# Optimization experiments

Hardware: AMD Instinct MI355X
Metric: run time of the kernel (lower is better)

The kernel has to match this reference:

```python
import jax, jax.numpy as jnp
import numpy as np

N_NODES = 100000
EMB = 256
HID = 64
N_REL = 5
N_EDGES = 3200000
BATCH = 16384


def _rgcn_conv(x, W, root, b, src, dst, etype):
    # PyG RGCNConv with mean aggregation per relation:
    # out_i = sum_r mean_{j in N_r(i)} x_j @ W_r + x_i @ root + b
    N = x.shape[0]
    R = W.shape[0]
    h = jnp.einsum('ni,rio->rno', x, W)          # [R, N, O] per-relation transforms
    m = h[etype, src]                            # [E, O] per-edge messages
    seg = dst * R + etype                        # combined (node, relation) segment id
    sums = jax.ops.segment_sum(m, seg, num_segments=N * R)
    cnt = jax.ops.segment_sum(jnp.ones((m.shape[0],), dtype=x.dtype), seg,
                              num_segments=N * R)
    mean = sums / jnp.maximum(cnt, 1.0)[:, None]
    agg = mean.reshape(N, R, -1).sum(axis=1)     # sum over relations
    return agg + x @ root + b


def _merge(x1, x2, w1, b1, w2, b2):
    x = jnp.concatenate([x1, x2], axis=1)
    h = jax.nn.relu(x @ w1 + b1)
    return h @ w2 + b2                           # [B, 1] logits


def setup_inputs() -> dict:
    key = jax.random.key(0)
    ks = jax.random.split(key, 16)
    d = {}
    d['bill_id'] = jax.random.randint(ks[0], (BATCH,), 0, N_NODES)
    d['user1_id'] = jax.random.randint(ks[1], (BATCH,), 0, N_NODES)
    d['user2_id'] = jax.random.randint(ks[2], (BATCH,), 0, N_NODES)
    d['edge_index'] = jax.random.randint(ks[3], (2, N_EDGES), 0, N_NODES)
    d['edge_type'] = jax.random.randint(ks[4], (N_EDGES,), 0, N_REL)
    # learned params (xavier-ish scaling); linear weights stored as [in, out]
    d['users_feature'] = jax.random.normal(ks[5], (N_NODES, EMB), jnp.float32) * 0.06
    d['W1'] = jax.random.normal(ks[6], (N_REL, EMB, HID), jnp.float32) * 0.08
    d['root1'] = jax.random.normal(ks[7], (EMB, HID), jnp.float32) * 0.08
    d['b1'] = jnp.zeros((HID,), jnp.float32)
    d['W2'] = jax.random.normal(ks[8], (N_REL, HID, HID), jnp.float32) * 0.12
    d['root2'] = jax.random.normal(ks[9], (HID, HID), jnp.float32) * 0.12
    d['b2'] = jnp.zeros((HID,), jnp.float32)
    d['mfc1_w'] = jax.random.normal(ks[10], (2 * HID, HID), jnp.float32) * 0.1
    d['mfc1_b'] = jnp.zeros((HID,), jnp.float32)
    d['mfc2_w'] = jax.random.normal(ks[11], (HID, 1), jnp.float32) * 0.17
    d['mfc2_b'] = jnp.zeros((1,), jnp.float32)
    return d


def reference(bill_id, user1_id, user2_id, edge_index, edge_type,
              users_feature, W1, root1, b1, W2, root2, b2,
              mfc1_w, mfc1_b, mfc2_w, mfc2_b):
    src, dst = edge_index[0], edge_index[1]
    x = jax.nn.relu(_rgcn_conv(users_feature, W1, root1, b1, src, dst, edge_type))
    nodes = _rgcn_conv(x, W2, root2, b2, src, dst, edge_type)  # [N, 64]
    bill = nodes[bill_id]
    u1 = nodes[user1_id]
    u2 = nodes[user2_id]
    pos = _merge(bill, u1, mfc1_w, mfc1_b, mfc2_w, mfc2_b)  # [B, 1]
    neg = _merge(bill, u2, mfc1_w, mfc1_b, mfc2_w, mfc2_b)
    z = jnp.concatenate([pos, neg], axis=0)
    t = jnp.concatenate([jnp.ones_like(pos), jnp.zeros_like(pos)], axis=0)
    # numerically stable BCE-with-logits, mean reduction
    bce = jnp.mean(jnp.maximum(z, 0.0) - z * t + jnp.log1p(jnp.exp(-jnp.abs(z))))
    pred = jnp.round(jax.nn.sigmoid(z))
    acc = jnp.mean((pred == t).astype(jnp.float32))
    return (bce, acc)
```

## Files before the change

### kernel.cpp

```cpp
#include <hip/hip_runtime.h>
#include <hip/hip_bf16.h>

#define N_NODES 100000
#define EMB 256
#define HID 64
#define N_REL 5
#define N_EDGES 3200000
#define BATCH 16384
#define NB 782
#define NWG1 256
#define CH 12500
#define LSEG 640
#define NSEG (N_NODES * N_REL)

typedef unsigned short u16;
typedef unsigned int u32;
typedef __attribute__((ext_vector_type(4))) float f32x4;
typedef __attribute__((ext_vector_type(8))) short short8;

__device__ __forceinline__ float bf2f(u16 u) {
    union { float f; u32 i; } v;
    v.i = ((u32)u) << 16;
    return v.f;
}
__device__ __forceinline__ u16 f2bf(float f) {
    union { float f; u32 i; } v;
    v.f = f;
    u32 r = v.i + 0x7fff + ((v.i >> 16) & 1);
    return (u16)(r >> 16);
}

__device__ __forceinline__ void gload_lds16(const void* g, void* l) {
    __builtin_amdgcn_global_load_lds(
        (const __attribute__((address_space(1))) unsigned int*)g,
        (__attribute__((address_space(3))) unsigned int*)l, 16, 0, 0);
}

__global__ __launch_bounds__(256) void bucket_hist(const int* __restrict__ dst,
                                                   int* __restrict__ hist) {
    __shared__ int hl[NB];
    const int tid = threadIdx.x;
    for (int i = tid; i < NB; i += 256) hl[i] = 0;
    __syncthreads();
    const int w = blockIdx.x;
    const int s = w * CH, e = s + CH;
    for (int i = s + tid; i < e; i += 256)
        atomicAdd(&hl[dst[i] >> 7], 1);
    __syncthreads();
    for (int i = tid; i < NB; i += 256) hist[w * NB + i] = hl[i];
}

__global__ void col_scan(int* __restrict__ hist, int* __restrict__ btot) {
    const int b = blockIdx.x;
    const int lane = threadIdx.x;
    int carry = 0;
    for (int c = 0; c < NWG1; c += 64) {
        int v = hist[(c + lane) * NB + b];
        int incl = v;
#pragma unroll
        for (int off = 1; off < 64; off <<= 1) {
            int t = __shfl_up(incl, off);
            if (lane >= off) incl += t;
        }
        hist[(c + lane) * NB + b] = carry + (incl - v);
        carry += __shfl(incl, 63);
    }
    if (lane == 0) btot[b] = carry;
}

__global__ void btot_scan(const int* __restrict__ btot, int* __restrict__ boffs,
                          int* __restrict__ offs) {
    const int lane = threadIdx.x;
    int carry = 0;
    for (int c = 0; c < NB; c += 64) {
        int v = (c + lane < NB) ? btot[c + lane] : 0;
        int incl = v;
#pragma unroll
        for (int off = 1; off < 64; off <<= 1) {
            int t = __shfl_up(incl, off);
            if (lane >= off) incl += t;
        }
        if (c + lane < NB) boffs[c + lane] = carry + (incl - v);
        carry += __shfl(incl, 63);
    }
    if (lane == 0) {
        boffs[NB] = N_EDGES;
        offs[NSEG] = N_EDGES;
    }
}

__global__ __launch_bounds__(256) void bucket_scatter(
        const int* __restrict__ src, const int* __restrict__ dst,
        const int* __restrict__ et, const int* __restrict__ base,
        const int* __restrict__ boffs, u32* __restrict__ bucketed) {
    __shared__ int cur[NB];
    const int tid = threadIdx.x;
    const int w = blockIdx.x;
    for (int i = tid; i < NB; i += 256) cur[i] = boffs[i] + base[w * NB + i];
    __syncthreads();
    const int s = w * CH, e = s + CH;
    for (int i = s + tid; i < e; i += 256) {
        int d = dst[i];
        int b = d >> 7;
        u32 key = (u32)src[i] | ((u32)((d & 127) * 5 + et[i]) << 17);
        int pos = atomicAdd(&cur[b], 1);
        bucketed[pos] = key;
    }
}

__global__ __launch_bounds__(256) void seg_sort(
        const u32* __restrict__ keys, const int* __restrict__ boffs,
        int* __restrict__ offs, u32* __restrict__ soff) {
    __shared__ int cntl[LSEG];
    __shared__ int cur[LSEG];
    const int tid = threadIdx.x;
    const int b = blockIdx.x;
    const int s = boffs[b], e = boffs[b + 1];

    for (int i = tid; i < LSEG; i += 256) cntl[i] = 0;
    __syncthreads();
    for (int i = s + tid; i < e; i += 256)
        atomicAdd(&cntl[keys[i] >> 17], 1);
    __syncthreads();

    if (tid < 64) {
        int carry = 0;
        for (int c = 0; c < LSEG; c += 64) {
            int v = cntl[c + tid];
            int incl = v;
#pragma unroll
            for (int off = 1; off < 64; off <<= 1) {
                int t = __shfl_up(incl, off);
                if (tid >= off) incl += t;
            }
            cur[c + tid] = carry + (incl - v);
            carry += __shfl(incl, 63);
        }
    }
    __syncthreads();

    const int segbase = b * LSEG;
    for (int i = tid; i < LSEG; i += 256)
        if (segbase + i < NSEG) offs[segbase + i] = s + cur[i];
    __syncthreads();

    for (int i = s + tid; i < e; i += 256) {
        u32 key = keys[i];
        u32 lseg = key >> 17;
        int pos = s + atomicAdd(&cur[lseg], 1);
        u32 q = (lseg * 52429u) >> 18;
        u32 rel = lseg - q * 5u;
        soff[pos] = (key & 0x1FFFF) * 384u + rel * 64u;
    }
}

__global__ void build_bt(const float* __restrict__ W, const float* __restrict__ root,
                         int K, u16* __restrict__ BT) {
    int idx = blockIdx.x * blockDim.x + threadIdx.x;
    if (idx >= 384 * K) return;
    int j = idx / K, k = idx - j * K;
    float v = (j < 320) ? W[((j >> 6) * K + k) * 64 + (j & 63)]
                        : root[k * 64 + (j & 63)];
    BT[idx] = f2bf(v);
}

template <int K, bool A_F32>
__global__ __launch_bounds__(256) void mfma_gemm(
        const void* __restrict__ Av, const u16* __restrict__ BT,
        u16* __restrict__ C) {
    __shared__ __align__(16) u16 Al[128 * 64];
    __shared__ __align__(16) u16 Bl[128 * 64];
    const int tid  = threadIdx.x;
    const int lane = tid & 63;
    const int wave = tid >> 6;
    const int m0 = blockIdx.x * 128;
    const int n0 = blockIdx.y * 128;
    const int wr = (wave >> 1) * 64;
    const int wc = (wave & 1) * 64;
    const int l15 = lane & 15;
    const int lg  = lane >> 4;

    f32x4 acc[4][4];
#pragma unroll
    for (int i = 0; i < 4; ++i)
#pragma unroll
        for (int j = 0; j < 4; ++j) {
            f32x4 z = {0.f, 0.f, 0.f, 0.f};
            acc[i][j] = z;
        }

    for (int k0 = 0; k0 < K; k0 += 64) {
#pragma unroll
        for (int i = 0; i < 4; ++i) {
            int c = wave * 4 + i;
            int row = c * 8 + (lane >> 3);
            int kk  = (lane & 7) * 8;
            gload_lds16(BT + (size_t)(n0 + row) * K + k0 + kk, &Bl[c * 512]);
        }
        if (A_F32) {
            const float* Af = (const float*)Av;
#pragma unroll
            for (int p = 0; p < 8; ++p) {
                int f = p * 1024 + tid * 4;
                int row = f >> 6;
                int col = f & 63;
                int gr = m0 + row;
                if (gr > N_NODES - 1) gr = N_NODES - 1;
                float4 v = *(const float4*)(Af + (size_t)gr * K + k0 + col);
                ushort4 o;
                o.x = f2bf(v.x); o.y = f2bf(v.y); o.z = f2bf(v.z); o.w = f2bf(v.w);
                *(ushort4*)&Al[row * 64 + col] = o;
            }
        } else {
            const u16* Ab = (const u16*)Av;
#pragma unroll
            for (int i = 0; i < 4; ++i) {
                int c = wave * 4 + i;
                int row = c * 8 + (lane >> 3);
                int kk  = (lane & 7) * 8;
                gload_lds16(Ab + (size_t)(m0 + row) * K + k0 + kk, &Al[c * 512]);
            }
        }
        __syncthreads();

#pragma unroll
        for (int kk = 0; kk < 64; kk += 32) {
            short8 af[4], bf[4];
#pragma unroll
            for (int f = 0; f < 4; ++f) {
                af[f] = *(const short8*)&Al[(wr + f * 16 + l15) * 64 + kk + lg * 8];
                bf[f] = *(const short8*)&Bl[(wc + f * 16 + l15) * 64 + kk + lg * 8];
            }
#pragma unroll
            for (int fm = 0; fm < 4; ++fm)
#pragma unroll
                for (int fn = 0; fn < 4; ++fn)
                    acc[fm][fn] = __builtin_amdgcn_mfma_f32_16x16x32_bf16(
                        af[fm], bf[fn], acc[fm][fn], 0, 0, 0);
        }
        __syncthreads();
    }

#pragma unroll
    for (int fm = 0; fm < 4; ++fm) {
        int rbase = m0 + wr + fm * 16 + lg * 4;
#pragma unroll
        for (int i = 0; i < 4; ++i) {
            int r = rbase + i;
            if (r < N_NODES) {
#pragma unroll
                for (int fn = 0; fn < 4; ++fn)
                    C[(size_t)r * 384 + n0 + wc + fn * 16 + l15] = f2bf(acc[fm][fn][i]);
            }
        }
    }
}

template <bool RELU>
__global__ __launch_bounds__(256) void agg_rl(
        const u16* __restrict__ h, const u32* __restrict__ soff,
        const int* __restrict__ offs, const float* __restrict__ bias,
        u16* __restrict__ out) {
    const int lane = threadIdx.x & 63;
    const int d = (blockIdx.x * blockDim.x + threadIdx.x) >> 6;
    if (d >= N_NODES) return;

    const int o0 = offs[d * 5 + 0], o1 = offs[d * 5 + 1], o2 = offs[d * 5 + 2];
    const int o3 = offs[d * 5 + 3], o4 = offs[d * 5 + 4], o5 = offs[d * 5 + 5];
    const float i0 = 1.f / (float)max(o1 - o0, 1);
    const float i1 = 1.f / (float)max(o2 - o1, 1);
    const float i2 = 1.f / (float)max(o3 - o2, 1);
    const float i3 = 1.f / (float)max(o4 - o3, 1);
    const float i4 = 1.f / (float)max(o5 - o4, 1);

    const u16* hl = h + lane;
    float acc0 = bf2f(h[(size_t)d * 384 + 320 + lane]) + bias[lane];
    float acc1 = 0.f;

    for (int base = o0; base < o5; base += 64) {
        const int idx = base + lane;
        const u32 voff = soff[min(idx, o5 - 1)];
        float wv = idx < o1 ? i0 : idx < o2 ? i1 : idx < o3 ? i2
                 : idx < o4 ? i3 : i4;
        if (idx >= o5) wv = 0.f;
        const int m = min(64, o5 - base);
        for (int j = 0; j < m; j += 8) {
#pragma unroll
            for (int jj = 0; jj < 8; jj += 2) {
                int  offa = __builtin_amdgcn_readlane((int)voff, j + jj);
                int  wa_i = __builtin_amdgcn_readlane((int)__float_as_uint(wv), j + jj);
                int  offb = __builtin_amdgcn_readlane((int)voff, j + jj + 1);
                int  wb_i = __builtin_amdgcn_readlane((int)__float_as_uint(wv), j + jj + 1);
                acc0 += bf2f(hl[(u32)offa]) * __uint_as_float((u32)wa_i);
                acc1 += bf2f(hl[(u32)offb]) * __uint_as_float((u32)wb_i);
            }
        }
    }
    float acc = acc0 + acc1;
    if (RELU) acc = fmaxf(acc, 0.f);
    out[(size_t)d * 64 + lane] = f2bf(acc);
}

__global__ __launch_bounds__(256) void loss_kernel(
        const u16* __restrict__ nodes, const int* __restrict__ bill,
        const int* __restrict__ u1, const int* __restrict__ u2,
        const float* __restrict__ w1, const float* __restrict__ b1,
        const float* __restrict__ w2, const float* __restrict__ b2,
        float* __restrict__ out) {
    __shared__ float Wl[128 * 64];
    __shared__ float red[2][4];
    for (int j = threadIdx.x; j < 128 * 16; j += 256)
        ((float4*)Wl)[j] = ((const float4*)w1)[j];
    __syncthreads();

    const int lane = threadIdx.x & 63;
    const int wv   = threadIdx.x >> 6;
    const int gw   = blockIdx.x * 4 + wv;
    const int nw   = gridDim.x * 4;

    const float bias1 = b1[lane];
    const float w2l   = w2[lane];
    const float bias2 = b2[0];

    float bce_acc = 0.f, corr_acc = 0.f;
    for (int s = gw; s < BATCH; s += nw) {
        const u16* xb  = nodes + (size_t)bill[s] * 64;
        const u16* xu1 = nodes + (size_t)u1[s] * 64;
        const u16* xu2 = nodes + (size_t)u2[s] * 64;
        float hb = bias1, h1 = 0.f, h2 = 0.f;
#pragma unroll 8
        for (int i = 0; i < 64; ++i) {
            float wb = Wl[i * 64 + lane];
            float wu = Wl[(64 + i) * 64 + lane];
            hb += bf2f(xb[i]) * wb;
            h1 += bf2f(xu1[i]) * wu;
            h2 += bf2f(xu2[i]) * wu;
        }
        float p1 = fmaxf(hb + h1, 0.f) * w2l;
        float p2 = fmaxf(hb + h2, 0.f) * w2l;
#pragma unroll
        for (int off = 32; off > 0; off >>= 1) {
            p1 += __shfl_down(p1, off);
            p2 += __shfl_down(p2, off);
        }
        if (lane == 0) {
            float z1 = p1 + bias2;
            float z2 = p2 + bias2;
            bce_acc += fmaxf(z1, 0.f) - z1 + log1pf(expf(-fabsf(z1)));
            bce_acc += fmaxf(z2, 0.f)      + log1pf(expf(-fabsf(z2)));
            corr_acc += (z1 > 0.f) ? 1.f : 0.f;
            corr_acc += (z2 > 0.f) ? 0.f : 1.f;
        }
    }
    if (lane == 0) { red[0][wv] = bce_acc; red[1][wv] = corr_acc; }
    __syncthreads();
    if (threadIdx.x == 0) {
        const float scale = 1.f / (2.f * BATCH);
        atomicAdd(&out[0], (red[0][0] + red[0][1] + red[0][2] + red[0][3]) * scale);
        atomicAdd(&out[1], (red[1][0] + red[1][1] + red[1][2] + red[1][3]) * scale);
    }
}

extern "C" void kernel_launch(void* const* d_in, const int* in_sizes, int n_in,
                              void* d_out, int out_size, void* d_ws, size_t ws_size,
                              hipStream_t stream) {
    const int*   bill  = (const int*)d_in[0];
    const int*   u1    = (const int*)d_in[1];
    const int*   u2    = (const int*)d_in[2];
    const int*   ei    = (const int*)d_in[3];
    const int*   et    = (const int*)d_in[4];
    const float* uf    = (const float*)d_in[5];
    const float* W1    = (const float*)d_in[6];
    const float* root1 = (const float*)d_in[7];
    const float* b1    = (const float*)d_in[8];
    const float* W2    = (const float*)d_in[9];
    const float* root2 = (const float*)d_in[10];
    const float* b2    = (const float*)d_in[11];
    const float* m1w   = (const float*)d_in[12];
    const float* m1b   = (const float*)d_in[13];
    const float* m2w   = (const float*)d_in[14];
    const float* m2b   = (const float*)d_in[15];
    float* out = (float*)d_out;

    char* ws = (char*)d_ws;
    u16* h_all    = (u16*)(ws);
    u32* sorted   = (u32*)(ws + 76800000);
    u32* bucketed = (u32*)(ws + 89600000);
    u16* xbuf     = (u16*)(ws + 89600000);
    int* hist     = (int*)(ws + 102400000);
    int* btot     = (int*)(ws + 103200768);
    int* boffs    = (int*)(ws + 103203896);
    int* offs     = (int*)(ws + 103207040);
    u16* BT1      = (u16*)(ws + 105207056);
    u16* BT2      = (u16*)(ws + 105403664);
    if (ws_size < 105452816) return;

    const int* src = ei;
    const int* dst = ei + N_EDGES;

    hipMemsetAsync(d_out, 0, 2 * sizeof(float), stream);

    bucket_hist<<<NWG1, 256, 0, stream>>>(dst, hist);
    col_scan<<<NB, 64, 0, stream>>>(hist, btot);
    btot_scan<<<1, 64, 0, stream>>>(btot, boffs, offs);
    bucket_scatter<<<NWG1, 256, 0, stream>>>(src, dst, et, hist, boffs, bucketed);
    seg_sort<<<NB, 256, 0, stream>>>(bucketed, boffs, offs, sorted);

    build_bt<<<(384 * EMB + 255) / 256, 256, 0, stream>>>(W1, root1, EMB, BT1);
    build_bt<<<(384 * HID + 255) / 256, 256, 0, stream>>>(W2, root2, HID, BT2);

    mfma_gemm<EMB, true><<<dim3(782, 3), 256, 0, stream>>>(uf, BT1, h_all);
    agg_rl<true><<<25000, 256, 0, stream>>>(h_all, sorted, offs, b1, xbuf);

    mfma_gemm<HID, false><<<dim3(782, 3), 256, 0, stream>>>(xbuf, BT2, h_all);
    agg_rl<false><<<25000, 256, 0, stream>>>(h_all, sorted, offs, b2, xbuf);

    loss_kernel<<<1024, 256, 0, stream>>>(xbuf, bill, u1, u2, m1w, m1b, m2w, m2b, out);
}
```

Before: 371.3 us.

## Compute full 384-column output per block and XOR-swizzle LDS tiles

The GEMM now has each 512-thread block compute all 384 output columns for its 128 rows, replacing the 3-way column-tiled grid. The A tile (the fp32 user features in layer 1) is therefore read and converted to bf16 once per row tile instead of three times. LDS rows are XOR-swizzled to cut bank conflicts on the MFMA fragment loads, and the fp32 A load now uses wider per-thread loads packed into 8-wide bf16 stores. In exchange, each block uses much more LDS and more accumulator registers per wave, which may reduce occupancy.

```diff
diff --git a/kernel.cpp b/kernel.cpp
--- a/kernel.cpp
+++ b/kernel.cpp
@@ -29,6 +29,14 @@
     u32 r = v.i + 0x7fff + ((v.i >> 16) & 1);
     return (u16)(r >> 16);
 }
+__device__ __forceinline__ short8 pack8(float4 a, float4 b) {
+    short8 r;
+    r[0] = (short)f2bf(a.x); r[1] = (short)f2bf(a.y);
+    r[2] = (short)f2bf(a.z); r[3] = (short)f2bf(a.w);
+    r[4] = (short)f2bf(b.x); r[5] = (short)f2bf(b.y);
+    r[6] = (short)f2bf(b.z); r[7] = (short)f2bf(b.w);
+    return r;
+}
 
 __device__ __forceinline__ void gload_lds16(const void* g, void* l) {
     __builtin_amdgcn_global_load_lds(
@@ -165,76 +173,76 @@
 }
 
 template <int K, bool A_F32>
-__global__ __launch_bounds__(256) void mfma_gemm(
+__global__ __launch_bounds__(512) void gemm384(
         const void* __restrict__ Av, const u16* __restrict__ BT,
         u16* __restrict__ C) {
     __shared__ __align__(16) u16 Al[128 * 64];
-    __shared__ __align__(16) u16 Bl[128 * 64];
+    __shared__ __align__(16) u16 Bl[384 * 64];
     const int tid  = threadIdx.x;
     const int lane = tid & 63;
-    const int wave = tid >> 6;
+    const int w    = tid >> 6;
     const int m0 = blockIdx.x * 128;
-    const int n0 = blockIdx.y * 128;
-    const int wr = (wave >> 1) * 64;
-    const int wc = (wave & 1) * 64;
+    const int wr = (w >> 2) * 64;
+    const int wc = (w & 3) * 96;
     const int l15 = lane & 15;
     const int lg  = lane >> 4;
 
-    f32x4 acc[4][4];
+    f32x4 acc[4][6];
 #pragma unroll
     for (int i = 0; i < 4; ++i)
 #pragma unroll
-        for (int j = 0; j < 4; ++j) {
+        for (int j = 0; j < 6; ++j) {
             f32x4 z = {0.f, 0.f, 0.f, 0.f};
             acc[i][j] = z;
         }
 
     for (int k0 = 0; k0 < K; k0 += 64) {
 #pragma unroll
-        for (int i = 0; i < 4; ++i) {
-            int c = wave * 4 + i;
-            int row = c * 8 + (lane >> 3);
-            int kk  = (lane & 7) * 8;
-            gload_lds16(BT + (size_t)(n0 + row) * K + k0 + kk, &Bl[c * 512]);
+        for (int j = 0; j < 6; ++j) {
+            int c = (j * 8 + w) * 64 + lane;
+            int row = c >> 3, sub = c & 7;
+            gload_lds16(BT + (size_t)row * K + k0 + ((sub ^ (row & 7)) * 8),
+                        &Bl[(j * 8 + w) * 512]);
         }
         if (A_F32) {
             const float* Af = (const float*)Av;
-#pragma unroll
-            for (int p = 0; p < 8; ++p) {
-                int f = p * 1024 + tid * 4;
-                int row = f >> 6;
-                int col = f & 63;
-                int gr = m0 + row;
-                if (gr > N_NODES - 1) gr = N_NODES - 1;
-                float4 v = *(const float4*)(Af + (size_t)gr * K + k0 + col);
-                ushort4 o;
-                o.x = f2bf(v.x); o.y = f2bf(v.y); o.z = f2bf(v.z); o.w = f2bf(v.w);
-                *(ushort4*)&Al[row * 64 + col] = o;
-            }
+            int row = tid >> 2;
+            int q0  = (tid & 3) * 2;
+            int grow = min(m0 + row, N_NODES - 1);
+            const float4* p = (const float4*)(Af + (size_t)grow * K + k0 + q0 * 8);
+            float4 v0 = p[0], v1 = p[1], v2 = p[2], v3 = p[3];
+            *(short8*)&Al[row * 64 + ((q0 ^ (row & 7)) * 8)]       = pack8(v0, v1);
+            *(short8*)&Al[row * 64 + (((q0 + 1) ^ (row & 7)) * 8)] = pack8(v2, v3);
         } else {
             const u16* Ab = (const u16*)Av;
 #pragma unroll
-            for (int i = 0; i < 4; ++i) {
-                int c = wave * 4 + i;
-                int row = c * 8 + (lane >> 3);
-                int kk  = (lane & 7) * 8;
-                gload_lds16(Ab + (size_t)(m0 + row) * K + k0 + kk, &Al[c * 512]);
+            for (int i = 0; i < 2; ++i) {
+                int c = (i * 8 + w) * 64 + lane;
+                int row = c >> 3, sub = c & 7;
+                gload_lds16(Ab + (size_t)(m0 + row) * K + k0 + ((sub ^ (row & 7)) * 8),
+                            &Al[(i * 8 + w) * 512]);
             }
         }
         __syncthreads();
 
 #pragma unroll
         for (int kk = 0; kk < 64; kk += 32) {
-            short8 af[4], bf[4];
+            const int ch = (kk >> 3) + lg;
+            short8 af[4], bf[6];
 #pragma unroll
             for (int f = 0; f < 4; ++f) {
-                af[f] = *(const short8*)&Al[(wr + f * 16 + l15) * 64 + kk + lg * 8];
-                bf[f] = *(const short8*)&Bl[(wc + f * 16 + l15) * 64 + kk + lg * 8];
+                int row = wr + f * 16 + l15;
+                af[f] = *(const short8*)&Al[row * 64 + ((ch ^ (row & 7)) * 8)];
+            }
+#pragma unroll
+            for (int f = 0; f < 6; ++f) {
+                int col = wc + f * 16 + l15;
+                bf[f] = *(const short8*)&Bl[col * 64 + ((ch ^ (col & 7)) * 8)];
             }
 #pragma unroll
             for (int fm = 0; fm < 4; ++fm)
 #pragma unroll
-                for (int fn = 0; fn < 4; ++fn)
+                for (int fn = 0; fn < 6; ++fn)
                     acc[fm][fn] = __builtin_amdgcn_mfma_f32_16x16x32_bf16(
                         af[fm], bf[fn], acc[fm][fn], 0, 0, 0);
         }
@@ -249,8 +257,8 @@
             int r = rbase + i;
             if (r < N_NODES) {
 #pragma unroll
-                for (int fn = 0; fn < 4; ++fn)
-                    C[(size_t)r * 384 + n0 + wc + fn * 16 + l15] = f2bf(acc[fm][fn][i]);
+                for (int fn = 0; fn < 6; ++fn)
+                    C[(size_t)r * 384 + wc + fn * 16 + l15] = f2bf(acc[fm][fn][i]);
             }
         }
     }
@@ -409,10 +417,10 @@
     build_bt<<<(384 * EMB + 255) / 256, 256, 0, stream>>>(W1, root1, EMB, BT1);
     build_bt<<<(384 * HID + 255) / 256, 256, 0, stream>>>(W2, root2, HID, BT2);
 
-    mfma_gemm<EMB, true><<<dim3(782, 3), 256, 0, stream>>>(uf, BT1, h_all);
+    gemm384<EMB, true><<<782, 512, 0, stream>>>(uf, BT1, h_all);
     agg_rl<true><<<25000, 256, 0, stream>>>(h_all, sorted, offs, b1, xbuf);
 
-    mfma_gemm<HID, false><<<dim3(782, 3), 256, 0, stream>>>(xbuf, BT2, h_all);
+    gemm384<HID, false><<<782, 512, 0, stream>>>(xbuf, BT2, h_all);
     agg_rl<false><<<25000, 256, 0, stream>>>(h_all, sorted, offs, b2, xbuf);
 
     loss_kernel<<<1024, 256, 0, stream>>>(xbuf, bill, u1, u2, m1w, m1b, m2w, m2b, out);
```

Result: no change. 377.8 us (+1.7%).
